# Performance work log

Measured on AMD Instinct MI355X. Metric: run time of the kernel, lower is better.

The kernel has to match this reference:

```python
import jax, jax.numpy as jnp
import numpy as np
from jax import lax

BN_EPS = 1e-5


def conv_bn_relu(x, W, g, b, m, v):
    # 3x3 conv, pad=1, stride=1, no bias; then inference-mode BN; then ReLU
    y = lax.conv_general_dilated(x, W, (1, 1), 'SAME',
                                 dimension_numbers=('NCHW', 'OIHW', 'NCHW'))
    scale = g / jnp.sqrt(v + BN_EPS)
    y = y * scale[None, :, None, None] + (b - m * scale)[None, :, None, None]
    return jax.nn.relu(y)


def shifted_windows(y, d, pad_val):
    # y: [n,c,h,w] -> [k*k, n, c, h, w] of all spatial shifts within radius d
    n, c, h, w = y.shape
    yp = jnp.pad(y, ((0, 0), (0, 0), (d, d), (d, d)), constant_values=pad_val)
    k = 2 * d + 1
    return jnp.stack([yp[:, :, i:i + h, j:j + w] for i in range(k) for j in range(k)], axis=0)


def setup_inputs() -> dict:
    key = jax.random.key(0)
    ks = jax.random.split(key, 16)
    n_clip, n, C_in, H, W = 2, 2, 512, 64, 64
    emb_dim, fc_dim, num_class = 256, 128, 124

    def bn_params(k, c):
        k1, k2, k3, k4 = jax.random.split(k, 4)
        return (jax.random.uniform(k1, (c,)) + 0.5,
                jax.random.normal(k2, (c,)) * 0.1,
                jax.random.normal(k3, (c,)) * 0.1,
                jax.random.uniform(k4, (c,)) + 0.5)

    emb_g, emb_b, emb_m, emb_v = bn_params(ks[0], emb_dim)
    emb2_g, emb2_b, emb2_m, emb2_v = bn_params(ks[1], fc_dim)
    return {
        'clip_embs': jax.random.normal(ks[2], (n_clip * n, C_in, H, W), dtype=jnp.float32),
        'clip_num': 2,
        'emb_W': jax.random.normal(ks[3], (emb_dim, C_in, 3, 3), dtype=jnp.float32) * 0.02,
        'emb_g': emb_g, 'emb_b': emb_b, 'emb_m': emb_m, 'emb_v': emb_v,
        'emb2_W': jax.random.normal(ks[4], (fc_dim, C_in, 3, 3), dtype=jnp.float32) * 0.02,
        'emb2_g': emb2_g, 'emb2_b': emb2_b, 'emb2_m': emb2_m, 'emb2_v': emb2_v,
        'last_W': jax.random.normal(ks[5], (num_class, emb_dim, 1, 1), dtype=jnp.float32) * 0.05,
        'last_b': jnp.zeros((num_class,), dtype=jnp.float32),
    }


MAX_DISTANCES = (2,)
TEMP = 1.0


def reference(clip_embs, clip_num, emb_W, emb_g, emb_b, emb_m, emb_v,
              emb2_W, emb2_g, emb2_b, emb2_m, emb2_v, last_W, last_b):
    # emb_2 features used for the local cost volume (fc_dim channels)
    clip_emb2 = conv_bn_relu(clip_embs, emb2_W, emb2_g, emb2_b, emb2_m, emb2_v)
    chunks2 = jnp.split(clip_emb2, clip_num, axis=0)
    c2 = chunks2[-1]                      # current frame, [n, fc_dim, h, w]
    others2 = chunks2[:-1]

    x2 = jnp.sum(c2 * c2, axis=1)         # [n,h,w]

    all_weights = []                       # per other clip: per max_distance softmax weights
    for other in others2:
        y2 = jnp.sum(other * other, axis=1, keepdims=True)  # [n,1,h,w]
        w_list = []
        for d in MAX_DISTANCES:
            k = 2 * d + 1
            y_sh = shifted_windows(other, d, 0.0)            # [k2,n,c,h,w]
            y2_sh = shifted_windows(y2, d, 1e20)[:, :, 0]    # [k2,n,h,w]
            cross = jnp.einsum('nchw,onchw->onhw', c2, y_sh)
            dist = x2[None] + y2_sh - 2.0 * cross            # [k2,n,h,w] squared L2
            # distsoftmax branch: softmax over the k*k window of 1/(dist*temp+1e-5)
            w_ = jax.nn.softmax(1.0 / (dist * TEMP + 1e-5), axis=0)
            w_list.append(w_)
        all_weights.append(w_list)

    # emb features (emb_dim channels) that get warped
    clip_emb_s = conv_bn_relu(clip_embs, emb_W, emb_g, emb_b, emb_m, emb_v)
    chunks_s = jnp.split(clip_emb_s, clip_num, axis=0)
    c_img = chunks_s[-1]                   # [n, emb_dim, h, w]
    others_s = chunks_s[:-1]

    final_emb = [c_img]
    for other, w_list in zip(others_s, all_weights):
        warp_fs = []
        for d, w_ in zip(MAX_DISTANCES, w_list):
            k = 2 * d + 1
            o_sh = shifted_windows(other, d, 0.0)            # [k2,n,c,h,w]
            # weighted sum over window, then avgpool over k*k -> divide by k*k
            warp = jnp.einsum('onchw,onhw->nchw', o_sh, w_) / (k * k)
            warp_fs.append(warp)
        final_emb.append(jnp.mean(jnp.stack(warp_fs, axis=-1), axis=-1))

    # linear_combine=False: mean over the clip embeddings
    final_fea = jnp.mean(jnp.stack(final_emb, axis=-1), axis=-1)

    # last_layer: dropout (eval -> identity) + 1x1 conv
    logits = jnp.einsum('nchw,oc->nohw', final_fea, last_W[:, :, 0, 0]) + last_b[None, :, None, None]
    x = jax.nn.log_softmax(logits, axis=1)
    return (x, clip_emb2)
```

## Files before the change

### kernel.cpp

```cpp
#include <hip/hip_runtime.h>
#include <hip/hip_bf16.h>
#include <stdint.h>


typedef float v4f __attribute__((ext_vector_type(4)));
typedef __bf16 v8bf __attribute__((ext_vector_type(8)));
typedef unsigned short u16;
typedef unsigned int u32;
typedef u16 u16x8 __attribute__((ext_vector_type(8)));

constexpr size_t XH_OFF  = 0;
constexpr size_t XH_BYTES = (size_t)4*66*66*512*2;
constexpr size_t WT_OFF  = XH_OFF + XH_BYTES;
constexpr size_t WT_BYTES = (size_t)9*16*24*64*8*2;
constexpr size_t FS_OFF  = WT_OFF + WT_BYTES;
constexpr size_t FS_BYTES = (size_t)4*68*68*256*2;
constexpr size_t F2_OFF  = FS_OFF + FS_BYTES;
constexpr size_t F2_BYTES = (size_t)4*68*68*128*4;
constexpr size_t Y2_OFF  = F2_OFF + F2_BYTES;
constexpr size_t Y2_BYTES = (size_t)2*68*68*4;
constexpr size_t FEA_OFF = Y2_OFF + Y2_BYTES;
constexpr size_t FEA_BYTES = (size_t)2*4096*256*2;
constexpr size_t WL_OFF  = FEA_OFF + FEA_BYTES;
constexpr size_t WL_BYTES = (size_t)128*256*2;
constexpr size_t SC_OFF  = WL_OFF + WL_BYTES;
constexpr size_t WS_TOTAL = SC_OFF + 768*4;

__device__ __forceinline__ float bf2f(u16 h) { return __uint_as_float(((u32)h) << 16); }
__device__ __forceinline__ u16 f2bf(float f) {
  u32 u = __float_as_uint(f);
  return (u16)((u + 0x7fffu + ((u >> 16) & 1u)) >> 16);
}

__device__ __forceinline__ void gld16(const void* g, const void* l) {
  __builtin_amdgcn_global_load_lds(
      (const __attribute__((address_space(1))) void*)(uintptr_t)g,
      (__attribute__((address_space(3))) void*)(u32)(uintptr_t)l,
      16, 0, 0);
}

__global__ __launch_bounds__(256) void k_prep(const float* __restrict__ X,
                       const float* __restrict__ embW, const float* __restrict__ emb2W,
                       const float* __restrict__ eg, const float* __restrict__ eb,
                       const float* __restrict__ em, const float* __restrict__ ev,
                       const float* __restrict__ e2g, const float* __restrict__ e2b,
                       const float* __restrict__ e2m, const float* __restrict__ e2v,
                       const float* __restrict__ lw,
                       u16* __restrict__ Xh, u16* __restrict__ Wf,
                       u16* __restrict__ Fs, float* __restrict__ F2,
                       float* __restrict__ Y2, u16* __restrict__ Wl,
                       float* __restrict__ sc, float* __restrict__ bi) {
  __shared__ __align__(16) char shbuf[18688];
  const int bid = blockIdx.x;
  const int tid = threadIdx.x;
  if (bid < 256) {
    const u32 N0 = 4u * 260u * 64u;
    const u32 N1 = 4u * 528u * 32u;
    const u32 N2 = 4u * 528u * 32u;
    const u32 N3 = 2u * 68u * 68u;
    const u32 N4 = 4096u;
    const u32 N5 = 384u;
    const u32 TOT = N0 + N1 + N2 + N3 + N4 + N5;
    const u16x8 z8 = {0,0,0,0,0,0,0,0};
    for (u32 i = bid * 256u + tid; i < TOT; i += 65536u) {
      if (i < N0) {
        const u32 img = i / (260u * 64u);
        const u32 rem = i - img * (260u * 64u);
        const u32 r = rem >> 6, ch8 = rem & 63u;
        u32 prow, pcol;
        if (r < 132u) { prow = (r >= 66u) ? 65u : 0u; pcol = r - ((r >= 66u) ? 66u : 0u); }
        else { const u32 rr = r - 132u; prow = 1u + (rr >> 1); pcol = (rr & 1u) * 65u; }
        *(u16x8*)(Xh + ((size_t)((img * 66u + prow) * 66u + pcol)) * 512u + ch8 * 8u) = z8;
      } else if (i < N0 + N1 + N2) {
        const bool isF2 = (i >= N0 + N1);
        const u32 j = isF2 ? (i - N0 - N1) : (i - N0);
        const u32 img = j / (528u * 32u);
        const u32 rem = j - img * (528u * 32u);
        const u32 r = rem >> 5, cg = rem & 31u;
        u32 prow, pcol;
        if (r < 272u) { const u32 q = r / 68u; prow = (q < 2u) ? q : q + 64u; pcol = r - q * 68u; }
        else { const u32 rr = r - 272u; prow = 2u + (rr >> 2); const u32 c = rr & 3u; pcol = (c < 2u) ? c : c + 64u; }
        if (isF2) {
          const float4 zf = {0.f, 0.f, 0.f, 0.f};
          *(float4*)(F2 + ((size_t)((img * 68u + prow) * 68u + pcol)) * 128u + cg * 4u) = zf;
        } else {
          *(u16x8*)(Fs + ((size_t)((img * 68u + prow) * 68u + pcol)) * 256u + cg * 8u) = z8;
        }
      } else if (i < N0 + N1 + N2 + N3) {
        const u32 j = i - N0 - N1 - N2;
        const u32 n = j / 4624u, rc = j - n * 4624u;
        const u32 rr = rc / 68u, cc = rc - rr * 68u;
        const bool interior = (rr >= 2u && rr < 66u && cc >= 2u && cc < 66u);
        Y2[j] = interior ? 0.f : 1e20f;
      } else if (i < N0 + N1 + N2 + N3 + N4) {
        const u32 j = i - N0 - N1 - N2 - N3;
        const u32 row = j >> 5, c8 = (j & 31u) * 8u;
        u16x8 o;
        #pragma unroll
        for (int k = 0; k < 8; ++k) o[k] = (row < 124u) ? f2bf(lw[row * 256u + c8 + k]) : (u16)0;
        *(u16x8*)(Wl + (size_t)row * 256u + c8) = o;
      } else {
        const u32 id = i - N0 - N1 - N2 - N3 - N4;
        float g, b, m, v;
        if (id < 256u) { g = eg[id]; b = eb[id]; m = em[id]; v = ev[id]; }
        else { const u32 q = id - 256u; g = e2g[q]; b = e2b[q]; m = e2m[q]; v = e2v[q]; }
        const float s = g / sqrtf(v + 1e-5f);
        sc[id] = s;
        bi[id] = b - m * s;
      }
    }
  } else if (bid < 768) {
    float* tile = (float*)shbuf;
    const int b2 = bid - 256;
    const int n = b2 >> 7;
    const int rem = b2 & 127;
    const int h = rem >> 1, chalf = rem & 1;
    const int wq = tid >> 6, wcol = tid & 63;
    #pragma unroll 1
    for (int it = 0; it < 4; ++it) {
      const int c0 = chalf * 256 + it * 64;
      __syncthreads();
      #pragma unroll
      for (int i = 0; i < 16; ++i) {
        const int cl = i * 4 + wq;
        tile[cl * 65 + wcol] = X[((size_t)(n * 512 + c0 + cl)) * 4096 + h * 64 + wcol];
      }
      __syncthreads();
      const int w = tid >> 2, cg = tid & 3;
      u16x8 a, b;
      #pragma unroll
      for (int j = 0; j < 8; ++j) a[j] = f2bf(tile[(cg * 16 + j) * 65 + w]);
      #pragma unroll
      for (int j = 0; j < 8; ++j) b[j] = f2bf(tile[(cg * 16 + 8 + j) * 65 + w]);
      u16* dst = Xh + ((size_t)((n * 66 + h + 1) * 66 + (w + 1))) * 512 + c0 + cg * 16;
      *(u16x8*)dst = a;
      *((u16x8*)dst + 1) = b;
    }
  } else {
    float* row = (float*)shbuf;
    const int oc = bid - 768;
    const float* src = (oc < 256) ? (embW + (size_t)oc * 4608) : (emb2W + (size_t)(oc - 256) * 4608);
    for (int i = tid; i < 4608; i += 256) row[i] = src[i];
    __syncthreads();
    const int cc = tid >> 4;
    const int slot = (tid >> 2) & 3;
    const int e = 2 * (tid & 3);
    const int r = oc & 15, ocb = oc >> 4;
    #pragma unroll
    for (int pos = 0; pos < 9; ++pos) {
      const u32 pk = (u32)f2bf(row[(2 * tid) * 9 + pos]) | ((u32)f2bf(row[(2 * tid + 1) * 9 + pos]) << 16);
      *(u32*)(Wf + ((size_t)((pos * 16 + cc) * 24 + ocb)) * 512 + (slot * 16 + r) * 8 + e) = pk;
    }
  }
}

__global__ __launch_bounds__(256) void k_conv(const u16* __restrict__ Xh, const u16* __restrict__ Wf,
                                              const float* __restrict__ sc, const float* __restrict__ bi,
                                              float* __restrict__ out2, float* __restrict__ F2,
                                              u16* __restrict__ Fs, float* __restrict__ Y2) {
  __shared__ __align__(16) char lds[42496];
  const int tid = threadIdx.x;
  const int wv = tid >> 6, lane = tid & 63;
  const int octile = blockIdx.x >> 7;
  const int rest = blockIdx.x & 127;
  const int n = rest >> 5, pt = rest & 31;
  const int h0 = pt * 2;
  const int ocb0 = octile * 4;
  const int pxrow = wv >> 1;
  const int pxc0 = (wv & 1) * 32;

  float* scl = (float*)(lds + 41984);
  float* bil = scl + 64;
  if (tid < 64) { scl[tid] = sc[octile * 64 + tid]; bil[tid] = bi[octile * 64 + tid]; }

  const u16* xbase = Xh + (size_t)n * 66 * 66 * 512;
  int bofs[5];
  #pragma unroll
  for (int k = 0; k < 5; ++k) {
    const int idx = k * 256 + tid;
    if (idx < 1056) {
      const int col = idx >> 2;
      const int ssrc = (idx & 3) ^ ((col >> 1) & 3);
      const int imgrow = col / 66, c = col - imgrow * 66;
      bofs[k] = ((h0 + imgrow) * 66 + c) * 512 + ssrc * 8;
    } else bofs[k] = 0;
  }

  auto stageA = [&](int pos, int cc, int buf) {
    gld16(Wf + ((size_t)((pos * 16 + cc) * 24 + ocb0)) * 512 + tid * 8, lds + buf * 4096 + tid * 16);
  };
  auto stageB = [&](int cc, int buf) {
    char* base = lds + 8192 + buf * 16896;
    #pragma unroll
    for (int k = 0; k < 4; ++k)
      gld16(xbase + bofs[k] + cc * 32, base + k * 4096 + tid * 16);
    if (tid < 32) gld16(xbase + bofs[4] + cc * 32, base + 16384 + tid * 16);
  };

  v4f acc[4][2];
  #pragma unroll
  for (int mt = 0; mt < 4; ++mt) { acc[mt][0] = (v4f){0,0,0,0}; acc[mt][1] = (v4f){0,0,0,0}; }

  int bA = 0, bB = 0;
  stageB(0, 0);
  stageA(0, 0, 0);
  __syncthreads();

  const int r0 = lane & 15;
  const int slotb = lane >> 4;
  const char* ldsB = lds + 8192;

  #pragma unroll 1
  for (int cc = 0; cc < 16; ++cc) {
    #pragma unroll
    for (int pos = 0; pos < 9; ++pos) {
      const int ky = pos / 3, kx = pos % 3;
      if (pos < 8) {
        stageA(pos + 1, cc, bA ^ 1);
      } else if (cc < 15) {
        stageB(cc + 1, bB ^ 1);
        stageA(0, cc + 1, bA ^ 1);
      }
      v8bf af[4], bfr[2];
      const char* pA = lds + bA * 4096 + lane * 16;
      #pragma unroll
      for (int mt = 0; mt < 4; ++mt) af[mt] = *(const v8bf*)(pA + mt * 1024);
      #pragma unroll
      for (int nt = 0; nt < 2; ++nt) {
        const int rb = (pxrow + ky) * 66 + pxc0 + nt * 16 + r0 + kx;
        bfr[nt] = *(const v8bf*)(ldsB + bB * 16896 + rb * 64 + ((slotb ^ ((rb >> 1) & 3)) << 4));
      }
      #pragma unroll
      for (int mt = 0; mt < 4; ++mt)
        #pragma unroll
        for (int nt = 0; nt < 2; ++nt)
          acc[mt][nt] = __builtin_amdgcn_mfma_f32_16x16x32_bf16(af[mt], bfr[nt], acc[mt][nt], 0, 0, 0);
      __syncthreads();
      bA ^= 1;
      if (pos == 8) bB ^= 1;
    }
  }

  const int q4 = (lane >> 4) << 2;
  float vals[4][2][4];
  #pragma unroll
  for (int mt = 0; mt < 4; ++mt) {
    const int ocb = mt * 16 + q4;
    #pragma unroll
    for (int j = 0; j < 4; ++j) {
      const float s = scl[ocb + j], tt = bil[ocb + j];
      #pragma unroll
      for (int nt = 0; nt < 2; ++nt) vals[mt][nt][j] = fmaxf(fmaf(acc[mt][nt][j], s, tt), 0.f);
    }
  }

  if (octile < 4) {
    u16* T = (u16*)lds;
    #pragma unroll
    for (int mt = 0; mt < 4; ++mt)
      #pragma unroll
      for (int nt = 0; nt < 2; ++nt) {
        const int p = pxrow * 64 + pxc0 + nt * 16 + r0;
        #pragma unroll
        for (int jj = 0; jj < 2; ++jj) {
          const int c = mt * 16 + q4 + 2 * jj;
          *(u32*)(T + p * 64 + (((c >> 3) ^ (p & 7)) << 3) + (c & 7)) =
              (u32)f2bf(vals[mt][nt][2 * jj]) | ((u32)f2bf(vals[mt][nt][2 * jj + 1]) << 16);
        }
      }
    __syncthreads();
    const int p = tid >> 1, half = tid & 1;
    u16* dst = Fs + ((size_t)((n * 68 + h0 + (p >> 6) + 2) * 68 + (p & 63) + 2)) * 256 + octile * 64 + half * 32;
    #pragma unroll
    for (int i = 0; i < 4; ++i) {
      const int cs = half * 4 + i;
      *(u16x8*)(dst + i * 8) = *(const u16x8*)(T + p * 64 + ((cs ^ (p & 7)) << 3));
    }
  } else {
    #pragma unroll
    for (int mt = 0; mt < 4; ++mt)
      #pragma unroll
      for (int j = 0; j < 4; ++j) {
        const int ocl = (octile - 4) * 64 + mt * 16 + q4 + j;
        float* orow = out2 + ((size_t)(n * 128 + ocl)) * 4096 + (h0 + pxrow) * 64 + pxc0;
        orow[r0] = vals[mt][0][j];
        orow[16 + r0] = vals[mt][1][j];
      }
    if (n < 2) {
      #pragma unroll
      for (int nt = 0; nt < 2; ++nt) {
        float s = 0.f;
        #pragma unroll
        for (int mt = 0; mt < 4; ++mt)
          #pragma unroll
          for (int j = 0; j < 4; ++j) s = fmaf(vals[mt][nt][j], vals[mt][nt][j], s);
        s += __shfl_xor(s, 16);
        s += __shfl_xor(s, 32);
        if ((lane >> 4) == 0)
          atomicAdd(&Y2[(size_t)(n * 68 + h0 + pxrow + 2) * 68 + pxc0 + nt * 16 + r0 + 2], s);
      }
    }
    float* T = (float*)lds;
    #pragma unroll
    for (int mt = 0; mt < 4; ++mt)
      #pragma unroll
      for (int nt = 0; nt < 2; ++nt) {
        const int p = pxrow * 64 + pxc0 + nt * 16 + r0;
        #pragma unroll
        for (int j = 0; j < 4; ++j) {
          const int c = mt * 16 + q4 + j;
          T[p * 64 + (((c >> 2) ^ (p & 15)) << 2) + (c & 3)] = vals[mt][nt][j];
        }
      }
    __syncthreads();
    const int p = tid >> 1, half = tid & 1;
    float* dst = F2 + ((size_t)((n * 68 + h0 + (p >> 6) + 2) * 68 + (p & 63) + 2)) * 128 + (octile - 4) * 64 + half * 32;
    #pragma unroll
    for (int i = 0; i < 8; ++i) {
      const int cs = half * 8 + i;
      *(float4*)(dst + i * 4) = *(const float4*)(T + p * 64 + ((cs ^ (p & 15)) << 2));
    }
  }
}

__global__ __launch_bounds__(256) void k_dw(const float* __restrict__ F2, const float* __restrict__ Y2,
                                            const u16* __restrict__ Fs, u16* __restrict__ Fea) {
  const int t = blockIdx.x * 256 + threadIdx.x;
  const int g = t & 15;
  const int px = t >> 4;
  const int n = px >> 12;
  const int p = px & 4095;
  const int h = p >> 6, w = p & 63;

  const float4* c2p = (const float4*)(F2 + ((size_t)(((n + 2) * 68 + h + 2) * 68 + (w + 2))) * 128 + g * 8);
  float4 c2v[2];
  float x2 = 0.f;
  #pragma unroll
  for (int i = 0; i < 2; ++i) {
    c2v[i] = c2p[i];
    x2 += c2v[i].x * c2v[i].x + c2v[i].y * c2v[i].y + c2v[i].z * c2v[i].z + c2v[i].w * c2v[i].w;
  }
  float cross[25];
  #pragma unroll
  for (int dy = 0; dy < 5; ++dy) {
    const float* rowp = F2 + ((size_t)((n * 68 + h + dy) * 68 + w)) * 128 + g * 8;
    #pragma unroll
    for (int dx = 0; dx < 5; ++dx) {
      const float4* wp = (const float4*)(rowp + dx * 128);
      float s = 0.f;
      #pragma unroll
      for (int i = 0; i < 2; ++i) {
        const float4 u = wp[i];
        s += c2v[i].x * u.x + c2v[i].y * u.y + c2v[i].z * u.z + c2v[i].w * u.w;
      }
      cross[dy * 5 + dx] = s;
    }
  }
  x2 += __shfl_xor(x2, 1); x2 += __shfl_xor(x2, 2); x2 += __shfl_xor(x2, 4); x2 += __shfl_xor(x2, 8);
  #pragma unroll
  for (int o = 0; o < 25; ++o) {
    cross[o] += __shfl_xor(cross[o], 1);
    cross[o] += __shfl_xor(cross[o], 2);
    cross[o] += __shfl_xor(cross[o], 4);
    cross[o] += __shfl_xor(cross[o], 8);
  }
  float wv[25], mx = -1e30f;
  #pragma unroll
  for (int dy = 0; dy < 5; ++dy)
    #pragma unroll
    for (int dx = 0; dx < 5; ++dx) {
      const int o = dy * 5 + dx;
      const float y2v = Y2[(size_t)(n * 68 + h + dy) * 68 + (w + dx)];
      const float dist = x2 + y2v - 2.f * cross[o];
      const float l = 1.f / (dist + 1e-5f);
      wv[o] = l;
      mx = fmaxf(mx, l);
    }
  float ssum = 0.f;
  #pragma unroll
  for (int o = 0; o < 25; ++o) { const float e = __expf(wv[o] - mx); wv[o] = e; ssum += e; }
  const float inv = 1.f / ssum;
  #pragma unroll
  for (int o = 0; o < 25; ++o) wv[o] *= inv;

  float facc[16];
  #pragma unroll
  for (int i = 0; i < 16; ++i) facc[i] = 0.f;
  #pragma unroll
  for (int dy = 0; dy < 5; ++dy) {
    const u16* rp = Fs + ((size_t)((n * 68 + h + dy) * 68 + w)) * 256 + g * 16;
    #pragma unroll
    for (int dx = 0; dx < 5; ++dx) {
      const float wt = wv[dy * 5 + dx];
      const u16x8* up = (const u16x8*)(rp + dx * 256);
      #pragma unroll
      for (int k = 0; k < 2; ++k) {
        const u16x8 u = up[k];
        #pragma unroll
        for (int j = 0; j < 8; ++j) facc[k * 8 + j] = fmaf(wt, bf2f(u[j]), facc[k * 8 + j]);
      }
    }
  }
  const u16x8* cip = (const u16x8*)(Fs + ((size_t)(((n + 2) * 68 + h + 2) * 68 + (w + 2))) * 256 + g * 16);
  u16x8* dp = (u16x8*)(Fea + ((size_t)(n * 4096 + p)) * 256 + g * 16);
  #pragma unroll
  for (int k = 0; k < 2; ++k) {
    const u16x8 cu = cip[k];
    u16x8 ou;
    #pragma unroll
    for (int j = 0; j < 8; ++j)
      ou[j] = f2bf(0.5f * (bf2f(cu[j]) + facc[k * 8 + j] * (1.f / 25.f)));
    dp[k] = ou;
  }
}

__global__ __launch_bounds__(128) void k_logits(const u16* __restrict__ Fea, const u16* __restrict__ Wl,
                                                const float* __restrict__ lb, float* __restrict__ xout) {
  const int wvi = threadIdx.x >> 6, lane = threadIdx.x & 63;
  const int wid = blockIdx.x * 2 + wvi;
  const int n = wid >> 8;
  const int p0 = (wid & 255) * 16;
  const int lp = lane & 15;
  const int kb = (lane >> 4) * 8;

  v4f acc[8];
  #pragma unroll
  for (int mt = 0; mt < 8; ++mt) acc[mt] = (v4f){0.f, 0.f, 0.f, 0.f};

  #pragma unroll
  for (int kc = 0; kc < 8; ++kc) {
    const v8bf b = *(const v8bf*)(Fea + ((size_t)(n * 4096 + p0 + lp)) * 256 + kc * 32 + kb);
    #pragma unroll
    for (int mt = 0; mt < 8; ++mt) {
      const v8bf a = *(const v8bf*)(Wl + ((size_t)(mt * 16 + lp)) * 256 + kc * 32 + kb);
      acc[mt] = __builtin_amdgcn_mfma_f32_16x16x32_bf16(a, b, acc[mt], 0, 0, 0);
    }
  }
  const int r0 = (lane >> 4) * 4;
  float v[8][4];
  float mx = -1e30f;
  #pragma unroll
  for (int mt = 0; mt < 8; ++mt)
    #pragma unroll
    for (int j = 0; j < 4; ++j) {
      const int cls = mt * 16 + r0 + j;
      const float val = (cls < 124) ? (acc[mt][j] + lb[cls]) : -1e30f;
      v[mt][j] = val;
      mx = fmaxf(mx, val);
    }
  mx = fmaxf(mx, __shfl_xor(mx, 16));
  mx = fmaxf(mx, __shfl_xor(mx, 32));
  float s = 0.f;
  #pragma unroll
  for (int mt = 0; mt < 8; ++mt)
    #pragma unroll
    for (int j = 0; j < 4; ++j) {
      const int cls = mt * 16 + r0 + j;
      if (cls < 124) s += __expf(v[mt][j] - mx);
    }
  s += __shfl_xor(s, 16);
  s += __shfl_xor(s, 32);
  const float lz = mx + logf(s);
  #pragma unroll
  for (int mt = 0; mt < 8; ++mt)
    #pragma unroll
    for (int j = 0; j < 4; ++j) {
      const int cls = mt * 16 + r0 + j;
      if (cls < 124)
        xout[((size_t)(n * 124 + cls)) * 4096 + p0 + lp] = v[mt][j] - lz;
    }
}

extern "C" void kernel_launch(void* const* d_in, const int* in_sizes, int n_in,
                              void* d_out, int out_size, void* d_ws, size_t ws_size,
                              hipStream_t stream) {
  (void)in_sizes; (void)n_in; (void)out_size;
  const float* clip  = (const float*)d_in[0];
  const float* embW  = (const float*)d_in[2];
  const float* eg    = (const float*)d_in[3];
  const float* eb    = (const float*)d_in[4];
  const float* em    = (const float*)d_in[5];
  const float* ev    = (const float*)d_in[6];
  const float* emb2W = (const float*)d_in[7];
  const float* e2g   = (const float*)d_in[8];
  const float* e2b   = (const float*)d_in[9];
  const float* e2m   = (const float*)d_in[10];
  const float* e2v   = (const float*)d_in[11];
  const float* lw    = (const float*)d_in[12];
  const float* lb    = (const float*)d_in[13];

  char* ws = (char*)d_ws;
  u16*   Xh  = (u16*)(ws + XH_OFF);
  u16*   Wf  = (u16*)(ws + WT_OFF);
  u16*   Fs  = (u16*)(ws + FS_OFF);
  float* F2  = (float*)(ws + F2_OFF);
  float* Y2  = (float*)(ws + Y2_OFF);
  u16*   Fea = (u16*)(ws + FEA_OFF);
  u16*   Wl  = (u16*)(ws + WL_OFF);
  float* sc  = (float*)(ws + SC_OFF);
  float* bi  = sc + 384;

  float* xout = (float*)d_out;
  float* out2 = xout + (size_t)2 * 124 * 64 * 64;

  if (ws_size < WS_TOTAL) return;

  k_prep<<<1152, 256, 0, stream>>>(clip, embW, emb2W, eg, eb, em, ev, e2g, e2b, e2m, e2v, lw,
                                   Xh, Wf, Fs, F2, Y2, Wl, sc, bi);
  k_conv<<<768, 256, 0, stream>>>(Xh, Wf, sc, bi, out2, F2, Fs, Y2);
  k_dw<<<512, 256, 0, stream>>>(F2, Y2, Fs, Fea);
  k_logits<<<256, 128, 0, stream>>>(Fea, Wl, lb, xout);
}
```

Before: 192.5 us.

## Double thread parallelism in k_dw and split-K the logits MFMA across waves

k_dw now assigns 32 threads per pixel instead of 16, so each thread handles 4 F2 channels and 8 Fs channels, and the grid doubles to 1024 blocks. This gives more parallelism and lowers register pressure, at the cost of one extra shuffle stage per reduction. k_logits splits the K dimension across two waves per pixel group and combines the partial accumulators through shared memory with a block barrier. That doubles the wave count for this small GEMM, but half the waves go idle during the softmax epilogue.

```diff
diff --git a/kernel.cpp b/kernel.cpp
--- a/kernel.cpp
+++ b/kernel.cpp
@@ -326,43 +326,33 @@
 __global__ __launch_bounds__(256) void k_dw(const float* __restrict__ F2, const float* __restrict__ Y2,
                                             const u16* __restrict__ Fs, u16* __restrict__ Fea) {
   const int t = blockIdx.x * 256 + threadIdx.x;
-  const int g = t & 15;
-  const int px = t >> 4;
+  const int g = t & 31;
+  const int px = t >> 5;
   const int n = px >> 12;
   const int p = px & 4095;
   const int h = p >> 6, w = p & 63;
 
-  const float4* c2p = (const float4*)(F2 + ((size_t)(((n + 2) * 68 + h + 2) * 68 + (w + 2))) * 128 + g * 8);
-  float4 c2v[2];
-  float x2 = 0.f;
-  #pragma unroll
-  for (int i = 0; i < 2; ++i) {
-    c2v[i] = c2p[i];
-    x2 += c2v[i].x * c2v[i].x + c2v[i].y * c2v[i].y + c2v[i].z * c2v[i].z + c2v[i].w * c2v[i].w;
-  }
+  const float4 c2v = *(const float4*)(F2 + ((size_t)(((n + 2) * 68 + h + 2) * 68 + (w + 2))) * 128 + g * 4);
+  float x2 = c2v.x * c2v.x + c2v.y * c2v.y + c2v.z * c2v.z + c2v.w * c2v.w;
   float cross[25];
   #pragma unroll
   for (int dy = 0; dy < 5; ++dy) {
-    const float* rowp = F2 + ((size_t)((n * 68 + h + dy) * 68 + w)) * 128 + g * 8;
+    const float* rowp = F2 + ((size_t)((n * 68 + h + dy) * 68 + w)) * 128 + g * 4;
     #pragma unroll
     for (int dx = 0; dx < 5; ++dx) {
-      const float4* wp = (const float4*)(rowp + dx * 128);
-      float s = 0.f;
-      #pragma unroll
-      for (int i = 0; i < 2; ++i) {
-        const float4 u = wp[i];
-        s += c2v[i].x * u.x + c2v[i].y * u.y + c2v[i].z * u.z + c2v[i].w * u.w;
-      }
-      cross[dy * 5 + dx] = s;
-    }
-  }
-  x2 += __shfl_xor(x2, 1); x2 += __shfl_xor(x2, 2); x2 += __shfl_xor(x2, 4); x2 += __shfl_xor(x2, 8);
+      const float4 u = *(const float4*)(rowp + dx * 128);
+      cross[dy * 5 + dx] = c2v.x * u.x + c2v.y * u.y + c2v.z * u.z + c2v.w * u.w;
+    }
+  }
+  x2 += __shfl_xor(x2, 1); x2 += __shfl_xor(x2, 2); x2 += __shfl_xor(x2, 4);
+  x2 += __shfl_xor(x2, 8); x2 += __shfl_xor(x2, 16);
   #pragma unroll
   for (int o = 0; o < 25; ++o) {
     cross[o] += __shfl_xor(cross[o], 1);
     cross[o] += __shfl_xor(cross[o], 2);
     cross[o] += __shfl_xor(cross[o], 4);
     cross[o] += __shfl_xor(cross[o], 8);
+    cross[o] += __shfl_xor(cross[o], 16);
   }
   float wv[25], mx = -1e30f;
   #pragma unroll
@@ -383,43 +373,37 @@
   #pragma unroll
   for (int o = 0; o < 25; ++o) wv[o] *= inv;
 
-  float facc[16];
-  #pragma unroll
-  for (int i = 0; i < 16; ++i) facc[i] = 0.f;
+  float facc[8];
+  #pragma unroll
+  for (int i = 0; i < 8; ++i) facc[i] = 0.f;
   #pragma unroll
   for (int dy = 0; dy < 5; ++dy) {
-    const u16* rp = Fs + ((size_t)((n * 68 + h + dy) * 68 + w)) * 256 + g * 16;
+    const u16* rp = Fs + ((size_t)((n * 68 + h + dy) * 68 + w)) * 256 + g * 8;
     #pragma unroll
     for (int dx = 0; dx < 5; ++dx) {
       const float wt = wv[dy * 5 + dx];
-      const u16x8* up = (const u16x8*)(rp + dx * 256);
-      #pragma unroll
-      for (int k = 0; k < 2; ++k) {
-        const u16x8 u = up[k];
-        #pragma unroll
-        for (int j = 0; j < 8; ++j) facc[k * 8 + j] = fmaf(wt, bf2f(u[j]), facc[k * 8 + j]);
-      }
-    }
-  }
-  const u16x8* cip = (const u16x8*)(Fs + ((size_t)(((n + 2) * 68 + h + 2) * 68 + (w + 2))) * 256 + g * 16);
-  u16x8* dp = (u16x8*)(Fea + ((size_t)(n * 4096 + p)) * 256 + g * 16);
-  #pragma unroll
-  for (int k = 0; k < 2; ++k) {
-    const u16x8 cu = cip[k];
-    u16x8 ou;
-    #pragma unroll
-    for (int j = 0; j < 8; ++j)
-      ou[j] = f2bf(0.5f * (bf2f(cu[j]) + facc[k * 8 + j] * (1.f / 25.f)));
-    dp[k] = ou;
-  }
-}
-
-__global__ __launch_bounds__(128) void k_logits(const u16* __restrict__ Fea, const u16* __restrict__ Wl,
+      const u16x8 u = *(const u16x8*)(rp + dx * 256);
+      #pragma unroll
+      for (int j = 0; j < 8; ++j) facc[j] = fmaf(wt, bf2f(u[j]), facc[j]);
+    }
+  }
+  const u16x8 cu = *(const u16x8*)(Fs + ((size_t)(((n + 2) * 68 + h + 2) * 68 + (w + 2))) * 256 + g * 8);
+  u16x8 ou;
+  #pragma unroll
+  for (int j = 0; j < 8; ++j)
+    ou[j] = f2bf(0.5f * (bf2f(cu[j]) + facc[j] * (1.f / 25.f)));
+  *(u16x8*)(Fea + ((size_t)(n * 4096 + p)) * 256 + g * 8) = ou;
+}
+
+__global__ __launch_bounds__(256) void k_logits(const u16* __restrict__ Fea, const u16* __restrict__ Wl,
                                                 const float* __restrict__ lb, float* __restrict__ xout) {
-  const int wvi = threadIdx.x >> 6, lane = threadIdx.x & 63;
-  const int wid = blockIdx.x * 2 + wvi;
-  const int n = wid >> 8;
-  const int p0 = (wid & 255) * 16;
+  __shared__ float part[2][8][64][4];
+  const int tid = threadIdx.x;
+  const int wvi = tid >> 6, lane = tid & 63;
+  const int pxg = wvi >> 1, kh = wvi & 1;
+  const int gid = blockIdx.x * 2 + pxg;
+  const int n = gid >> 8;
+  const int p0 = (gid & 255) * 16;
   const int lp = lane & 15;
   const int kb = (lane >> 4) * 8;
 
@@ -428,7 +412,8 @@
   for (int mt = 0; mt < 8; ++mt) acc[mt] = (v4f){0.f, 0.f, 0.f, 0.f};
 
   #pragma unroll
-  for (int kc = 0; kc < 8; ++kc) {
+  for (int ki = 0; ki < 4; ++ki) {
+    const int kc = kh * 4 + ki;
     const v8bf b = *(const v8bf*)(Fea + ((size_t)(n * 4096 + p0 + lp)) * 256 + kc * 32 + kb);
     #pragma unroll
     for (int mt = 0; mt < 8; ++mt) {
@@ -436,18 +421,28 @@
       acc[mt] = __builtin_amdgcn_mfma_f32_16x16x32_bf16(a, b, acc[mt], 0, 0, 0);
     }
   }
+  if (kh == 1) {
+    #pragma unroll
+    for (int mt = 0; mt < 8; ++mt)
+      *(v4f*)&part[pxg][mt][lane][0] = acc[mt];
+  }
+  __syncthreads();
+  if (kh == 1) return;
+
   const int r0 = (lane >> 4) * 4;
   float v[8][4];
   float mx = -1e30f;
   #pragma unroll
-  for (int mt = 0; mt < 8; ++mt)
+  for (int mt = 0; mt < 8; ++mt) {
+    const v4f o = *(const v4f*)&part[pxg][mt][lane][0];
     #pragma unroll
     for (int j = 0; j < 4; ++j) {
       const int cls = mt * 16 + r0 + j;
-      const float val = (cls < 124) ? (acc[mt][j] + lb[cls]) : -1e30f;
+      const float val = (cls < 124) ? (acc[mt][j] + o[j] + lb[cls]) : -1e30f;
       v[mt][j] = val;
       mx = fmaxf(mx, val);
     }
+  }
   mx = fmaxf(mx, __shfl_xor(mx, 16));
   mx = fmaxf(mx, __shfl_xor(mx, 32));
   float s = 0.f;
@@ -508,6 +503,6 @@
   k_prep<<<1152, 256, 0, stream>>>(clip, embW, emb2W, eg, eb, em, ev, e2g, e2b, e2m, e2v, lw,
                                    Xh, Wf, Fs, F2, Y2, Wl, sc, bi);
   k_conv<<<768, 256, 0, stream>>>(Xh, Wf, sc, bi, out2, F2, Fs, Y2);
-  k_dw<<<512, 256, 0, stream>>>(F2, Y2, Fs, Fea);
-  k_logits<<<256, 128, 0, stream>>>(Fea, Wl, lb, xout);
-}
+  k_dw<<<1024, 256, 0, stream>>>(F2, Y2, Fs, Fea);
+  k_logits<<<256, 256, 0, stream>>>(Fea, Wl, lb, xout);
+}
```

After: 192.8 us. About the same (+0.2%).
